# Kernel tuning notes

Hardware: AMD Instinct MI355X
Metric: run time of the kernel (lower is better)

## Reference

```python
import jax, jax.numpy as jnp
import numpy as np

B, QL, KVL = 4, 512, 4096
Q_DIM, KV_DIM = 1024, 768
QK_CH, V_CH, H = 1024, 1024, 8
DQK, DV = QK_CH // H, V_CH // H
LN_EPS = 1e-3  # keras LayerNormalization default epsilon


def layernorm(x, gamma, beta):
    mu = jnp.mean(x, axis=-1, keepdims=True)
    var = jnp.mean(jnp.square(x - mu), axis=-1, keepdims=True)
    return (x - mu) * jax.lax.rsqrt(var + LN_EPS) * gamma + beta


def setup_inputs() -> dict:
    key = jax.random.key(0)
    ks = jax.random.split(key, 8)
    s_q = 1.0 / np.sqrt(Q_DIM)
    s_kv = 1.0 / np.sqrt(KV_DIM)
    return {
        "hidden_states": jax.random.normal(ks[0], (B, QL, Q_DIM), jnp.float32),
        "inputs": jax.random.normal(ks[1], (B, KVL, KV_DIM), jnp.float32),
        "ln1_g": jnp.ones((Q_DIM,), jnp.float32),
        "ln1_b": jnp.zeros((Q_DIM,), jnp.float32),
        "ln2_g": jnp.ones((KV_DIM,), jnp.float32),
        "ln2_b": jnp.zeros((KV_DIM,), jnp.float32),
        "Wq": jax.random.normal(ks[2], (Q_DIM, QK_CH), jnp.float32) * s_q,
        "bq": jnp.zeros((QK_CH,), jnp.float32),
        "Wk": jax.random.normal(ks[3], (KV_DIM, QK_CH), jnp.float32) * s_kv,
        "bk": jnp.zeros((QK_CH,), jnp.float32),
        "Wv": jax.random.normal(ks[4], (KV_DIM, V_CH), jnp.float32) * s_kv,
        "bv": jnp.zeros((V_CH,), jnp.float32),
    }


def reference(hidden_states, inputs, ln1_g, ln1_b, ln2_g, ln2_b, Wq, bq, Wk, bk, Wv, bv):
    # LayerNorm latents and inputs (cross-attention path)
    hs = layernorm(hidden_states, ln1_g, ln1_b)   # [B, QL, Q_DIM]
    inp = layernorm(inputs, ln2_g, ln2_b)         # [B, KVL, KV_DIM]

    q = hs @ Wq + bq                               # [B, QL, QK_CH]
    k = inp @ Wk + bk                              # [B, KVL, QK_CH]
    v = inp @ Wv + bv                              # [B, KVL, V_CH]

    q = q.reshape(B, QL, H, DQK)
    k = k.reshape(B, KVL, H, DQK)
    v = v.reshape(B, KVL, H, DV)

    scores = jnp.einsum("bqhd,bkhd->bhqk", q, k) / jnp.sqrt(jnp.asarray(DQK, q.dtype))
    probs = jax.nn.softmax(scores, axis=-1)        # [B, H, QL, KVL]
    ctx = jnp.einsum("bhqk,bkhd->bqhd", probs, v)  # [B, QL, H, DV]
    return ctx.reshape(B, QL, H * DV)
```

## Files before the change

### kernel.cpp

```cpp
#include <hip/hip_runtime.h>
#include <hip/hip_bf16.h>
#include <stdint.h>

#define B_    4
#define QL_   512
#define KVL_  4096
#define QDIM  1024
#define KVDIM 768
#define NCH   1024
#define H_    8
#define DH    128
#define NROWS (B_ * H_ * QL_)
#define KVBLK 64
#define NS    4

typedef unsigned short ushort_t;
typedef __attribute__((ext_vector_type(8))) short bf16x8;
typedef __attribute__((ext_vector_type(4))) float f32x4;
typedef __attribute__((ext_vector_type(4))) unsigned short us4;

__device__ __forceinline__ ushort_t f2bf(float x){
  union { float f; unsigned u; } v; v.f = x;
  unsigned r = v.u + 0x7FFF + ((v.u >> 16) & 1);
  return (ushort_t)(r >> 16);
}

__device__ __forceinline__ void gload16(void* l, const void* g){
  __builtin_amdgcn_global_load_lds(
    (const __attribute__((address_space(1))) unsigned int*)g,
    (__attribute__((address_space(3))) unsigned int*)l, 16, 0, 0);
}

template<int D>
__global__ void ln_kernel(const float* __restrict__ x, const float* __restrict__ gamma,
                          const float* __restrict__ beta, ushort_t* __restrict__ out){
  int row = blockIdx.x;
  const float* xr = x + (size_t)row * D;
  ushort_t* orow = out + (size_t)row * D;
  int tid = threadIdx.x;
  constexpr int NPT = D / 256;
  float v[NPT];
  float s = 0.f, s2 = 0.f;
  #pragma unroll
  for (int k = 0; k < NPT; ++k){ v[k] = xr[tid + k*256]; s += v[k]; s2 += v[k]*v[k]; }
  #pragma unroll
  for (int m = 32; m; m >>= 1){ s += __shfl_xor(s, m); s2 += __shfl_xor(s2, m); }
  __shared__ float red[8];
  int w = tid >> 6;
  if ((tid & 63) == 0){ red[w] = s; red[4 + w] = s2; }
  __syncthreads();
  s  = red[0] + red[1] + red[2] + red[3];
  s2 = red[4] + red[5] + red[6] + red[7];
  float mu  = s / D;
  float var = s2 / D - mu * mu;
  float rs  = rsqrtf(var + 1e-3f);
  #pragma unroll
  for (int k = 0; k < NPT; ++k){
    int i = tid + k*256;
    orow[i] = f2bf((v[k] - mu) * rs * gamma[i] + beta[i]);
  }
}

__global__ void wtrans_kernel(const float* __restrict__ W, ushort_t* __restrict__ Wt,
                              int K, int N){
  __shared__ float t[32][33];
  int n0 = blockIdx.x * 32, k0 = blockIdx.y * 32;
  int tx = threadIdx.x & 31, ty = threadIdx.x >> 5;
  #pragma unroll
  for (int i = 0; i < 32; i += 8) t[ty + i][tx] = W[(size_t)(k0 + ty + i) * N + n0 + tx];
  __syncthreads();
  #pragma unroll
  for (int i = 0; i < 32; i += 8)
    Wt[(size_t)(n0 + ty + i) * K + k0 + tx] = f2bf(t[tx][ty + i]);
}

__global__ __launch_bounds__(256)
void gemm_kernel(const ushort_t* __restrict__ A, const ushort_t* __restrict__ Bw,
                 const float* __restrict__ bias, ushort_t* __restrict__ out,
                 int M, int K, float oscale){
  __shared__ __align__(16) ushort_t lds[3][2][4][128][8];
  int tid = threadIdx.x;
  int w = tid >> 6, lane = tid & 63;
  int m0 = blockIdx.x * 128, n0 = blockIdx.y * 128;
  int wr = w >> 1, wc = w & 1;
  int g = lane >> 4, j = lane & 15;
  f32x4 acc[4][4] = {};
  const int ksteps = K / 32;
  const ushort_t* Aw  = A  + (size_t)(m0 + lane) * K + w * 8;
  const ushort_t* Bww = Bw + (size_t)(n0 + lane) * K + w * 8;

  auto stage = [&](int buf, int ks){
    #pragma unroll
    for (int i = 0; i < 2; ++i){
      gload16(&lds[buf][0][w][i*64][0], Aw  + (size_t)i*64*K + ks*32);
      gload16(&lds[buf][1][w][i*64][0], Bww + (size_t)i*64*K + ks*32);
    }
  };

  stage(0, 0);
  stage(1, 1);
  asm volatile("s_waitcnt vmcnt(4)" ::: "memory");
  __builtin_amdgcn_s_barrier();
  __builtin_amdgcn_sched_barrier(0);

  int cur = 0;
  for (int ks = 0; ks < ksteps; ++ks){
    int nxt = cur + 2; if (nxt >= 3) nxt -= 3;
    bool pf = (ks + 2 < ksteps);
    if (pf) stage(nxt, ks + 2);
    bf16x8 af[4], bfr[4];
    #pragma unroll
    for (int mi = 0; mi < 4; ++mi) af[mi]  = *(const bf16x8*)&lds[cur][0][g][wr*64 + mi*16 + j][0];
    #pragma unroll
    for (int ni = 0; ni < 4; ++ni) bfr[ni] = *(const bf16x8*)&lds[cur][1][g][wc*64 + ni*16 + j][0];
    __builtin_amdgcn_s_setprio(1);
    #pragma unroll
    for (int mi = 0; mi < 4; ++mi)
      #pragma unroll
      for (int ni = 0; ni < 4; ++ni)
        acc[mi][ni] = __builtin_amdgcn_mfma_f32_16x16x32_bf16(af[mi], bfr[ni], acc[mi][ni], 0, 0, 0);
    __builtin_amdgcn_s_setprio(0);
    if (pf) asm volatile("s_waitcnt vmcnt(4)" ::: "memory");
    else    asm volatile("s_waitcnt vmcnt(0)" ::: "memory");
    __builtin_amdgcn_s_barrier();
    __builtin_amdgcn_sched_barrier(0);
    cur += 1; if (cur >= 3) cur -= 3;
  }

  #pragma unroll
  for (int mi = 0; mi < 4; ++mi){
    int row0 = m0 + wr*64 + mi*16 + g*4;
    #pragma unroll
    for (int ni = 0; ni < 4; ++ni){
      int col = n0 + wc*64 + ni*16 + j;
      float bs = bias[col];
      #pragma unroll
      for (int r = 0; r < 4; ++r)
        out[(size_t)(row0 + r) * NCH + col] = f2bf((acc[mi][ni][r] + bs) * oscale);
    }
  }
}

template<bool TRANSV>
__global__ __launch_bounds__(512, 2)
void gemm256_kernel(const ushort_t* __restrict__ A, const ushort_t* __restrict__ Bw,
                    const float* __restrict__ bias, ushort_t* __restrict__ out,
                    int M, int K, float oscale){
  __shared__ __align__(16) ushort_t lds[3][2][256][32];
  int tid = threadIdx.x;
  int w = tid >> 6, lane = tid & 63;
  int m0 = blockIdx.x * 256, n0 = blockIdx.y * 256;
  int wr = w >> 2, wc = w & 3;
  int g = lane >> 4, j = lane & 15;
  f32x4 acc[8][4] = {};
  const int ksteps = K / 32;
  int srow = tid >> 2, scolb = (tid & 3) * 8;
  const ushort_t* Asrc = A  + (size_t)(m0 + srow) * K + scolb;
  const ushort_t* Bsrc = Bw + (size_t)(n0 + srow) * K + scolb;

  auto stage = [&](int buf, int ks){
    char* la = (char*)&lds[buf][0][0][0] + tid * 16;
    char* lb = (char*)&lds[buf][1][0][0] + tid * 16;
    #pragma unroll
    for (int i = 0; i < 2; ++i){
      gload16(la + i*8192, Asrc + (size_t)(i*128)*K + ks*32);
      gload16(lb + i*8192, Bsrc + (size_t)(i*128)*K + ks*32);
    }
  };

  stage(0, 0);
  stage(1, 1);
  asm volatile("s_waitcnt vmcnt(4)" ::: "memory");
  __builtin_amdgcn_s_barrier();
  __builtin_amdgcn_sched_barrier(0);

  int cur = 0;
  for (int ks = 0; ks < ksteps; ++ks){
    int nxt = cur + 2; if (nxt >= 3) nxt -= 3;
    bool pf = (ks + 2 < ksteps);
    if (pf) stage(nxt, ks + 2);
    const char* La = (const char*)&lds[cur][0][0][0];
    const char* Lb = (const char*)&lds[cur][1][0][0];
    bf16x8 af[8], bfr[4];
    #pragma unroll
    for (int mi = 0; mi < 8; ++mi) af[mi]  = *(const bf16x8*)(La + ((wr*128 + mi*16 + j) << 6) + (g << 4));
    #pragma unroll
    for (int ni = 0; ni < 4; ++ni) bfr[ni] = *(const bf16x8*)(Lb + ((wc*64  + ni*16 + j) << 6) + (g << 4));
    __builtin_amdgcn_s_setprio(1);
    #pragma unroll
    for (int mi = 0; mi < 8; ++mi)
      #pragma unroll
      for (int ni = 0; ni < 4; ++ni)
        acc[mi][ni] = __builtin_amdgcn_mfma_f32_16x16x32_bf16(af[mi], bfr[ni], acc[mi][ni], 0, 0, 0);
    __builtin_amdgcn_s_setprio(0);
    if (pf) asm volatile("s_waitcnt vmcnt(4)" ::: "memory");
    else    asm volatile("s_waitcnt vmcnt(0)" ::: "memory");
    __builtin_amdgcn_s_barrier();
    __builtin_amdgcn_sched_barrier(0);
    cur += 1; if (cur >= 3) cur -= 3;
  }

  #pragma unroll
  for (int mi = 0; mi < 8; ++mi){
    int row0 = m0 + wr*128 + mi*16 + g*4;
    #pragma unroll
    for (int ni = 0; ni < 4; ++ni){
      int col = n0 + wc*64 + ni*16 + j;
      float bs = bias[col];
      if (!TRANSV){
        #pragma unroll
        for (int r = 0; r < 4; ++r)
          out[(size_t)(row0 + r) * NCH + col] = f2bf((acc[mi][ni][r] + bs) * oscale);
      } else {
        int bidx = row0 >> 12, kv = row0 & (KVL_ - 1);
        int h = col >> 7, dv = col & 127;
        int c = (kv & ~31) | (((kv & 15) >> 2) << 3) | (((kv >> 4) & 1) << 2);
        us4 pk;
        #pragma unroll
        for (int r = 0; r < 4; ++r) pk[r] = f2bf(acc[mi][ni][r] + bs);
        *(us4*)&out[((size_t)(bidx * H_ + h) * DH + dv) * KVL_ + c] = pk;
      }
    }
  }
}

__global__ __launch_bounds__(512, 4)
void attn_kernel(const ushort_t* __restrict__ Q, const ushort_t* __restrict__ Km,
                 const ushort_t* __restrict__ Vt, float* __restrict__ ctxp,
                 float* __restrict__ mlp){
  __shared__ __align__(16) ushort_t Kbuf[2][KVBLK][DH];
  __shared__ __align__(16) ushort_t Vbuf[2][DH][KVBLK];

  int bid = blockIdx.x;
  int xcd = bid & 7, slot = bid >> 3;
  int p   = xcd + 8 * (slot >> 2);
  int qb  = slot & 3;
  int bh  = p >> 2, sp = p & 3;
  int b = bh >> 3, h = bh & 7;

  int tid = threadIdx.x;
  int w = tid >> 6, lane = tid & 63;
  int g = lane >> 4, j = lane & 15;
  int qbase = qb * 128 + w * 16;

  bf16x8 qreg[4];
  {
    const ushort_t* Qb = Q + (size_t)(b * QL_ + qbase + j) * NCH + h * DH + g * 8;
    #pragma unroll
    for (int kb = 0; kb < 4; ++kb) qreg[kb] = *(const bf16x8*)(Qb + kb * 32);
  }

  f32x4 ctx[8] = {};
  float m_ = -1e30f, l_ = 0.f;

  const int kvbeg = sp * (KVL_ / NS);
  const char* Kg = (const char*)(Km + (size_t)b * KVL_ * NCH) + h * 256;
  const char* Vg = (const char*)(Vt + (size_t)(b * H_ + h) * DH * KVL_);

  auto stage = [&](int bi, int kv0){
    #pragma unroll
    for (int i = 0; i < 2; ++i){
      int lin = (i * 512 + tid) * 16;
      int sw  = lin ^ (((lin >> 8) & 7) << 4);
      gload16((char*)&Kbuf[bi][0][0] + lin,
              Kg + (size_t)(kv0 + (sw >> 8)) * 2048 + (sw & 255));
    }
    #pragma unroll
    for (int i = 0; i < 2; ++i){
      int lin = (i * 512 + tid) * 16;
      int sw  = lin ^ (((lin >> 7) & 7) << 4);
      gload16((char*)&Vbuf[bi][0][0] + lin,
              Vg + (size_t)(sw >> 7) * (KVL_ * 2) + kv0 * 2 + (sw & 127));
    }
  };

  const float THR = 11.5415603f;
  const int NCHUNK = (KVL_ / NS) / KVBLK;

  stage(0, kvbeg);
  __syncthreads();

  for (int c = 0; c < NCHUNK; ++c){
    int bi = c & 1;
    if (c + 1 < NCHUNK) stage(bi ^ 1, kvbeg + (c + 1) * KVBLK);

    const char* Kl = (const char*)&Kbuf[bi][0][0];
    const char* Vl = (const char*)&Vbuf[bi][0][0];

    f32x4 s[4] = {};
    __builtin_amdgcn_s_setprio(1);
    #pragma unroll
    for (int kf = 0; kf < 4; ++kf){
      #pragma unroll
      for (int kb = 0; kb < 4; ++kb){
        int off = (kf * 16 + j) * 256 + kb * 64 + g * 16;
        off ^= ((j & 7) << 4);
        s[kf] = __builtin_amdgcn_mfma_f32_16x16x32_bf16(
                  *(const bf16x8*)(Kl + off), qreg[kb], s[kf], 0, 0, 0);
      }
    }
    __builtin_amdgcn_s_setprio(0);

    float pm = s[0][0];
    #pragma unroll
    for (int kf = 0; kf < 4; ++kf)
      #pragma unroll
      for (int r = 0; r < 4; ++r) pm = fmaxf(pm, s[kf][r]);
    pm = fmaxf(pm, __shfl_xor(pm, 16));
    pm = fmaxf(pm, __shfl_xor(pm, 32));
    int ok = (pm - m_ <= THR);
    if (!__all(ok)){
      float mn = fmaxf(m_, pm);
      float cf = exp2f(m_ - mn);
      m_ = mn;
      l_ *= cf;
      float cfr[4];
      #pragma unroll
      for (int r = 0; r < 4; ++r) cfr[r] = __shfl(cf, g * 4 + r);
      #pragma unroll
      for (int df = 0; df < 8; ++df)
        #pragma unroll
        for (int r = 0; r < 4; ++r) ctx[df][r] *= cfr[r];
    }
    float rs = 0.f;
    #pragma unroll
    for (int kf = 0; kf < 4; ++kf)
      #pragma unroll
      for (int r = 0; r < 4; ++r){ s[kf][r] = exp2f(s[kf][r] - m_); rs += s[kf][r]; }
    rs += __shfl_xor(rs, 16);
    rs += __shfl_xor(rs, 32);
    l_ += rs;

    union { unsigned u[4]; bf16x8 v; } pa[2];
    #pragma unroll
    for (int kb = 0; kb < 2; ++kb){
      asm("v_cvt_pk_bf16_f32 %0, %1, %2" : "=v"(pa[kb].u[0]) : "v"(s[2*kb][0]),   "v"(s[2*kb][1]));
      asm("v_cvt_pk_bf16_f32 %0, %1, %2" : "=v"(pa[kb].u[1]) : "v"(s[2*kb][2]),   "v"(s[2*kb][3]));
      asm("v_cvt_pk_bf16_f32 %0, %1, %2" : "=v"(pa[kb].u[2]) : "v"(s[2*kb+1][0]), "v"(s[2*kb+1][1]));
      asm("v_cvt_pk_bf16_f32 %0, %1, %2" : "=v"(pa[kb].u[3]) : "v"(s[2*kb+1][2]), "v"(s[2*kb+1][3]));
    }

    __builtin_amdgcn_s_setprio(1);
    #pragma unroll
    for (int df = 0; df < 8; ++df){
      int off0 = (df * 16 + j) * 128 + g * 16;        int o0 = off0 ^ ((j & 7) << 4);
      int off1 = (df * 16 + j) * 128 + 64 + g * 16;   int o1 = off1 ^ ((j & 7) << 4);
      ctx[df] = __builtin_amdgcn_mfma_f32_16x16x32_bf16(pa[0].v, *(const bf16x8*)(Vl + o0), ctx[df], 0, 0, 0);
      ctx[df] = __builtin_amdgcn_mfma_f32_16x16x32_bf16(pa[1].v, *(const bf16x8*)(Vl + o1), ctx[df], 0, 0, 0);
    }
    __builtin_amdgcn_s_setprio(0);
    __syncthreads();
  }

  size_t prow0 = ((size_t)sp * 32 + bh) * QL_ + qbase;
  #pragma unroll
  for (int r = 0; r < 4; ++r){
    float* cp = ctxp + (prow0 + g * 4 + r) * DH;
    #pragma unroll
    for (int df = 0; df < 8; ++df) cp[df * 16 + j] = ctx[df][r];
  }
  if (g == 0){
    mlp[(prow0 + j) * 2]     = m_;
    mlp[(prow0 + j) * 2 + 1] = l_;
  }
}

__global__ __launch_bounds__(256)
void combine_kernel(const float* __restrict__ ctxp, const float* __restrict__ mlp,
                    float* __restrict__ out){
  int row = blockIdx.x * 4 + (threadIdx.x >> 6);
  int lane = threadIdx.x & 63;
  int b = row >> 12, h = (row >> 9) & 7, q = row & 511;
  float ms[NS], ls[NS];
  #pragma unroll
  for (int s = 0; s < NS; ++s){
    ms[s] = mlp[((size_t)(s * NROWS + row)) * 2];
    ls[s] = mlp[((size_t)(s * NROWS + row)) * 2 + 1];
  }
  float M = ms[0];
  #pragma unroll
  for (int s = 1; s < NS; ++s) M = fmaxf(M, ms[s]);
  float wgt[NS], L = 0.f;
  #pragma unroll
  for (int s = 0; s < NS; ++s){ wgt[s] = exp2f(ms[s] - M); L += ls[s] * wgt[s]; }
  float inv = 1.f / L;
  float ax = 0.f, ay = 0.f;
  #pragma unroll
  for (int s = 0; s < NS; ++s){
    const float* cp = ctxp + ((size_t)(s * NROWS + row)) * DH + lane * 2;
    ax += cp[0] * wgt[s]; ay += cp[1] * wgt[s];
  }
  float* op = out + ((size_t)(b * QL_ + q)) * NCH + h * DH + lane * 2;
  op[0] = ax * inv; op[1] = ay * inv;
}

extern "C" void kernel_launch(void* const* d_in, const int* in_sizes, int n_in,
                              void* d_out, int out_size, void* d_ws, size_t ws_size,
                              hipStream_t stream){
  const float* hs   = (const float*)d_in[0];
  const float* inp  = (const float*)d_in[1];
  const float* ln1g = (const float*)d_in[2];
  const float* ln1b = (const float*)d_in[3];
  const float* ln2g = (const float*)d_in[4];
  const float* ln2b = (const float*)d_in[5];
  const float* Wq   = (const float*)d_in[6];
  const float* bq   = (const float*)d_in[7];
  const float* Wk   = (const float*)d_in[8];
  const float* bk   = (const float*)d_in[9];
  const float* Wv   = (const float*)d_in[10];
  const float* bv   = (const float*)d_in[11];

  char* ws = (char*)d_ws;
  size_t off = 0;
  auto alloc = [&](size_t bytes){ void* pp = ws + off; off += (bytes + 255) & ~255ull; return pp; };
  ushort_t* Qm = (ushort_t*)alloc((size_t)2048 * 1024 * 2);
  ushort_t* Km = (ushort_t*)alloc((size_t)16384 * 1024 * 2);
  ushort_t* Vt = (ushort_t*)alloc((size_t)16384 * 1024 * 2);
  size_t base2 = off;
  ushort_t* hs_ln = (ushort_t*)alloc((size_t)2048 * 1024 * 2);
  ushort_t* in_ln = (ushort_t*)alloc((size_t)16384 * 768 * 2);
  ushort_t* Wqt   = (ushort_t*)alloc((size_t)1024 * 1024 * 2);
  ushort_t* Wkt   = (ushort_t*)alloc((size_t)1024 * 768 * 2);
  ushort_t* Wvt   = (ushort_t*)alloc((size_t)1024 * 768 * 2);
  off = base2;
  float* ctxp = (float*)alloc((size_t)NS * NROWS * DH * 4);
  float* mlp  = (float*)alloc((size_t)NS * NROWS * 2 * 4);

  const float QSC = 0.08838834764831845f * 1.4426950408889634f;

  ln_kernel<1024><<<2048, 256, 0, stream>>>(hs, ln1g, ln1b, hs_ln);
  ln_kernel<768><<<16384, 256, 0, stream>>>(inp, ln2g, ln2b, in_ln);
  wtrans_kernel<<<dim3(32, 32), 256, 0, stream>>>(Wq, Wqt, 1024, 1024);
  wtrans_kernel<<<dim3(32, 24), 256, 0, stream>>>(Wk, Wkt, 768, 1024);
  wtrans_kernel<<<dim3(32, 24), 256, 0, stream>>>(Wv, Wvt, 768, 1024);
  gemm_kernel<<<dim3(16, 8), 256, 0, stream>>>(hs_ln, Wqt, bq, Qm, 2048, 1024, QSC);
  gemm256_kernel<false><<<dim3(64, 4), 512, 0, stream>>>(in_ln, Wkt, bk, Km, 16384, 768, 1.0f);
  gemm256_kernel<true ><<<dim3(64, 4), 512, 0, stream>>>(in_ln, Wvt, bv, Vt, 16384, 768, 1.0f);
  attn_kernel<<<512, 512, 0, stream>>>(Qm, Km, Vt, ctxp, mlp);
  combine_kernel<<<NROWS / 4, 256, 0, stream>>>(ctxp, mlp, (float*)d_out);
}
```

Before: 175.3 us.

## Give each attention wave two query tiles and vectorize layernorm loads

The attention kernel drops from 512 to 256 threads per block, and each wave now handles two 16-row query groups. Each K and V fragment read from LDS is reused across two MFMAs, which halves LDS read traffic per unit of work. The cost is more registers per wave (two sets of ctx accumulators and softmax state) and fewer waves to hide latency. Separately, the layernorm kernel now does float4 loads and a packed bf16 store, with block size set to D/4 threads.

Result: no change. 176.4 us (+0.6%).

```diff
diff --git a/kernel.cpp b/kernel.cpp
--- a/kernel.cpp
+++ b/kernel.cpp
@@ -34,31 +34,31 @@
 template<int D>
 __global__ void ln_kernel(const float* __restrict__ x, const float* __restrict__ gamma,
                           const float* __restrict__ beta, ushort_t* __restrict__ out){
+  constexpr int NW = D / 256;
   int row = blockIdx.x;
-  const float* xr = x + (size_t)row * D;
-  ushort_t* orow = out + (size_t)row * D;
+  const f32x4* xr = (const f32x4*)(x + (size_t)row * D);
   int tid = threadIdx.x;
-  constexpr int NPT = D / 256;
-  float v[NPT];
-  float s = 0.f, s2 = 0.f;
-  #pragma unroll
-  for (int k = 0; k < NPT; ++k){ v[k] = xr[tid + k*256]; s += v[k]; s2 += v[k]*v[k]; }
+  f32x4 v = xr[tid];
+  float s  = v[0] + v[1] + v[2] + v[3];
+  float s2 = v[0]*v[0] + v[1]*v[1] + v[2]*v[2] + v[3]*v[3];
   #pragma unroll
   for (int m = 32; m; m >>= 1){ s += __shfl_xor(s, m); s2 += __shfl_xor(s2, m); }
-  __shared__ float red[8];
+  __shared__ float red[2 * NW];
   int w = tid >> 6;
-  if ((tid & 63) == 0){ red[w] = s; red[4 + w] = s2; }
+  if ((tid & 63) == 0){ red[w] = s; red[NW + w] = s2; }
   __syncthreads();
-  s  = red[0] + red[1] + red[2] + red[3];
-  s2 = red[4] + red[5] + red[6] + red[7];
+  s = 0.f; s2 = 0.f;
+  #pragma unroll
+  for (int i = 0; i < NW; ++i){ s += red[i]; s2 += red[NW + i]; }
   float mu  = s / D;
   float var = s2 / D - mu * mu;
   float rs  = rsqrtf(var + 1e-3f);
-  #pragma unroll
-  for (int k = 0; k < NPT; ++k){
-    int i = tid + k*256;
-    orow[i] = f2bf((v[k] - mu) * rs * gamma[i] + beta[i]);
-  }
+  f32x4 gm = ((const f32x4*)gamma)[tid];
+  f32x4 bt = ((const f32x4*)beta)[tid];
+  us4 o;
+  #pragma unroll
+  for (int e = 0; e < 4; ++e) o[e] = f2bf((v[e] - mu) * rs * gm[e] + bt[e]);
+  ((us4*)(out + (size_t)row * D))[tid] = o;
 }
 
 __global__ void wtrans_kernel(const float* __restrict__ W, ushort_t* __restrict__ Wt,
@@ -224,7 +224,7 @@
   }
 }
 
-__global__ __launch_bounds__(512, 4)
+__global__ __launch_bounds__(256, 2)
 void attn_kernel(const ushort_t* __restrict__ Q, const ushort_t* __restrict__ Km,
                  const ushort_t* __restrict__ Vt, float* __restrict__ ctxp,
                  float* __restrict__ mlp){
@@ -241,17 +241,18 @@
   int tid = threadIdx.x;
   int w = tid >> 6, lane = tid & 63;
   int g = lane >> 4, j = lane & 15;
-  int qbase = qb * 128 + w * 16;
-
-  bf16x8 qreg[4];
-  {
-    const ushort_t* Qb = Q + (size_t)(b * QL_ + qbase + j) * NCH + h * DH + g * 8;
-    #pragma unroll
-    for (int kb = 0; kb < 4; ++kb) qreg[kb] = *(const bf16x8*)(Qb + kb * 32);
-  }
-
-  f32x4 ctx[8] = {};
-  float m_ = -1e30f, l_ = 0.f;
+  int qbase = qb * 128 + w * 32;
+
+  bf16x8 qreg[2][4];
+  #pragma unroll
+  for (int qg = 0; qg < 2; ++qg){
+    const ushort_t* Qb = Q + (size_t)(b * QL_ + qbase + qg * 16 + j) * NCH + h * DH + g * 8;
+    #pragma unroll
+    for (int kb = 0; kb < 4; ++kb) qreg[qg][kb] = *(const bf16x8*)(Qb + kb * 32);
+  }
+
+  f32x4 ctx[2][8] = {};
+  float m_[2] = {-1e30f, -1e30f}, l_[2] = {0.f, 0.f};
 
   const int kvbeg = sp * (KVL_ / NS);
   const char* Kg = (const char*)(Km + (size_t)b * KVL_ * NCH) + h * 256;
@@ -259,15 +260,15 @@
 
   auto stage = [&](int bi, int kv0){
     #pragma unroll
-    for (int i = 0; i < 2; ++i){
-      int lin = (i * 512 + tid) * 16;
+    for (int i = 0; i < 4; ++i){
+      int lin = (i * 256 + tid) * 16;
       int sw  = lin ^ (((lin >> 8) & 7) << 4);
       gload16((char*)&Kbuf[bi][0][0] + lin,
               Kg + (size_t)(kv0 + (sw >> 8)) * 2048 + (sw & 255));
     }
     #pragma unroll
-    for (int i = 0; i < 2; ++i){
-      int lin = (i * 512 + tid) * 16;
+    for (int i = 0; i < 4; ++i){
+      int lin = (i * 256 + tid) * 16;
       int sw  = lin ^ (((lin >> 7) & 7) << 4);
       gload16((char*)&Vbuf[bi][0][0] + lin,
               Vg + (size_t)(sw >> 7) * (KVL_ * 2) + kv0 * 2 + (sw & 127));
@@ -287,7 +288,7 @@
     const char* Kl = (const char*)&Kbuf[bi][0][0];
     const char* Vl = (const char*)&Vbuf[bi][0][0];
 
-    f32x4 s[4] = {};
+    f32x4 s[2][4] = {};
     __builtin_amdgcn_s_setprio(1);
     #pragma unroll
     for (int kf = 0; kf < 4; ++kf){
@@ -295,49 +296,56 @@
       for (int kb = 0; kb < 4; ++kb){
         int off = (kf * 16 + j) * 256 + kb * 64 + g * 16;
         off ^= ((j & 7) << 4);
-        s[kf] = __builtin_amdgcn_mfma_f32_16x16x32_bf16(
-                  *(const bf16x8*)(Kl + off), qreg[kb], s[kf], 0, 0, 0);
+        bf16x8 kfrag = *(const bf16x8*)(Kl + off);
+        s[0][kf] = __builtin_amdgcn_mfma_f32_16x16x32_bf16(kfrag, qreg[0][kb], s[0][kf], 0, 0, 0);
+        s[1][kf] = __builtin_amdgcn_mfma_f32_16x16x32_bf16(kfrag, qreg[1][kb], s[1][kf], 0, 0, 0);
       }
     }
     __builtin_amdgcn_s_setprio(0);
 
-    float pm = s[0][0];
-    #pragma unroll
-    for (int kf = 0; kf < 4; ++kf)
-      #pragma unroll
-      for (int r = 0; r < 4; ++r) pm = fmaxf(pm, s[kf][r]);
-    pm = fmaxf(pm, __shfl_xor(pm, 16));
-    pm = fmaxf(pm, __shfl_xor(pm, 32));
-    int ok = (pm - m_ <= THR);
-    if (!__all(ok)){
-      float mn = fmaxf(m_, pm);
-      float cf = exp2f(m_ - mn);
-      m_ = mn;
-      l_ *= cf;
-      float cfr[4];
-      #pragma unroll
-      for (int r = 0; r < 4; ++r) cfr[r] = __shfl(cf, g * 4 + r);
-      #pragma unroll
-      for (int df = 0; df < 8; ++df)
+    union { unsigned u[4]; bf16x8 v; } pa[2][2];
+    #pragma unroll
+    for (int qg = 0; qg < 2; ++qg){
+      float t0 = fmaxf(fmaxf(s[qg][0][0], s[qg][0][1]), fmaxf(s[qg][0][2], s[qg][0][3]));
+      float t1 = fmaxf(fmaxf(s[qg][1][0], s[qg][1][1]), fmaxf(s[qg][1][2], s[qg][1][3]));
+      float t2 = fmaxf(fmaxf(s[qg][2][0], s[qg][2][1]), fmaxf(s[qg][2][2], s[qg][2][3]));
+      float t3 = fmaxf(fmaxf(s[qg][3][0], s[qg][3][1]), fmaxf(s[qg][3][2], s[qg][3][3]));
+      float pm = fmaxf(fmaxf(t0, t1), fmaxf(t2, t3));
+      pm = fmaxf(pm, __shfl_xor(pm, 16));
+      pm = fmaxf(pm, __shfl_xor(pm, 32));
+      int ok = (pm - m_[qg] <= THR);
+      if (!__all(ok)){
+        float mn = fmaxf(m_[qg], pm);
+        float cf = exp2f(m_[qg] - mn);
+        m_[qg] = mn;
+        l_[qg] *= cf;
+        float cfr[4];
         #pragma unroll
-        for (int r = 0; r < 4; ++r) ctx[df][r] *= cfr[r];
-    }
-    float rs = 0.f;
-    #pragma unroll
-    for (int kf = 0; kf < 4; ++kf)
-      #pragma unroll
-      for (int r = 0; r < 4; ++r){ s[kf][r] = exp2f(s[kf][r] - m_); rs += s[kf][r]; }
-    rs += __shfl_xor(rs, 16);
-    rs += __shfl_xor(rs, 32);
-    l_ += rs;
-
-    union { unsigned u[4]; bf16x8 v; } pa[2];
-    #pragma unroll
-    for (int kb = 0; kb < 2; ++kb){
-      asm("v_cvt_pk_bf16_f32 %0, %1, %2" : "=v"(pa[kb].u[0]) : "v"(s[2*kb][0]),   "v"(s[2*kb][1]));
-      asm("v_cvt_pk_bf16_f32 %0, %1, %2" : "=v"(pa[kb].u[1]) : "v"(s[2*kb][2]),   "v"(s[2*kb][3]));
-      asm("v_cvt_pk_bf16_f32 %0, %1, %2" : "=v"(pa[kb].u[2]) : "v"(s[2*kb+1][0]), "v"(s[2*kb+1][1]));
-      asm("v_cvt_pk_bf16_f32 %0, %1, %2" : "=v"(pa[kb].u[3]) : "v"(s[2*kb+1][2]), "v"(s[2*kb+1][3]));
+        for (int r = 0; r < 4; ++r) cfr[r] = __shfl(cf, g * 4 + r);
+        #pragma unroll
+        for (int df = 0; df < 8; ++df)
+          #pragma unroll
+          for (int r = 0; r < 4; ++r) ctx[qg][df][r] *= cfr[r];
+      }
+      float rs0 = 0.f, rs1 = 0.f;
+      #pragma unroll
+      for (int kf = 0; kf < 4; ++kf)
+        #pragma unroll
+        for (int r = 0; r < 4; ++r){
+          s[qg][kf][r] = exp2f(s[qg][kf][r] - m_[qg]);
+          if (kf < 2) rs0 += s[qg][kf][r]; else rs1 += s[qg][kf][r];
+        }
+      float rs = rs0 + rs1;
+      rs += __shfl_xor(rs, 16);
+      rs += __shfl_xor(rs, 32);
+      l_[qg] += rs;
+      #pragma unroll
+      for (int kb = 0; kb < 2; ++kb){
+        asm("v_cvt_pk_bf16_f32 %0, %1, %2" : "=v"(pa[qg][kb].u[0]) : "v"(s[qg][2*kb][0]),   "v"(s[qg][2*kb][1]));
+        asm("v_cvt_pk_bf16_f32 %0, %1, %2" : "=v"(pa[qg][kb].u[1]) : "v"(s[qg][2*kb][2]),   "v"(s[qg][2*kb][3]));
+        asm("v_cvt_pk_bf16_f32 %0, %1, %2" : "=v"(pa[qg][kb].u[2]) : "v"(s[qg][2*kb+1][0]), "v"(s[qg][2*kb+1][1]));
+        asm("v_cvt_pk_bf16_f32 %0, %1, %2" : "=v"(pa[qg][kb].u[3]) : "v"(s[qg][2*kb+1][2]), "v"(s[qg][2*kb+1][3]));
+      }
     }
 
     __builtin_amdgcn_s_setprio(1);
@@ -345,23 +353,30 @@
     for (int df = 0; df < 8; ++df){
       int off0 = (df * 16 + j) * 128 + g * 16;        int o0 = off0 ^ ((j & 7) << 4);
       int off1 = (df * 16 + j) * 128 + 64 + g * 16;   int o1 = off1 ^ ((j & 7) << 4);
-      ctx[df] = __builtin_amdgcn_mfma_f32_16x16x32_bf16(pa[0].v, *(const bf16x8*)(Vl + o0), ctx[df], 0, 0, 0);
-      ctx[df] = __builtin_amdgcn_mfma_f32_16x16x32_bf16(pa[1].v, *(const bf16x8*)(Vl + o1), ctx[df], 0, 0, 0);
+      bf16x8 v0 = *(const bf16x8*)(Vl + o0);
+      bf16x8 v1 = *(const bf16x8*)(Vl + o1);
+      ctx[0][df] = __builtin_amdgcn_mfma_f32_16x16x32_bf16(pa[0][0].v, v0, ctx[0][df], 0, 0, 0);
+      ctx[0][df] = __builtin_amdgcn_mfma_f32_16x16x32_bf16(pa[0][1].v, v1, ctx[0][df], 0, 0, 0);
+      ctx[1][df] = __builtin_amdgcn_mfma_f32_16x16x32_bf16(pa[1][0].v, v0, ctx[1][df], 0, 0, 0);
+      ctx[1][df] = __builtin_amdgcn_mfma_f32_16x16x32_bf16(pa[1][1].v, v1, ctx[1][df], 0, 0, 0);
     }
     __builtin_amdgcn_s_setprio(0);
     __syncthreads();
   }
 
-  size_t prow0 = ((size_t)sp * 32 + bh) * QL_ + qbase;
-  #pragma unroll
-  for (int r = 0; r < 4; ++r){
-    float* cp = ctxp + (prow0 + g * 4 + r) * DH;
-    #pragma unroll
-    for (int df = 0; df < 8; ++df) cp[df * 16 + j] = ctx[df][r];
-  }
-  if (g == 0){
-    mlp[(prow0 + j) * 2]     = m_;
-    mlp[(prow0 + j) * 2 + 1] = l_;
+  #pragma unroll
+  for (int qg = 0; qg < 2; ++qg){
+    size_t prow0 = ((size_t)sp * 32 + bh) * QL_ + qbase + qg * 16;
+    #pragma unroll
+    for (int r = 0; r < 4; ++r){
+      float* cp = ctxp + (prow0 + g * 4 + r) * DH;
+      #pragma unroll
+      for (int df = 0; df < 8; ++df) cp[df * 16 + j] = ctx[qg][df][r];
+    }
+    if (g == 0){
+      mlp[(prow0 + j) * 2]     = m_[qg];
+      mlp[(prow0 + j) * 2 + 1] = l_[qg];
+    }
   }
 }
 
@@ -429,13 +444,13 @@
   const float QSC = 0.08838834764831845f * 1.4426950408889634f;
 
   ln_kernel<1024><<<2048, 256, 0, stream>>>(hs, ln1g, ln1b, hs_ln);
-  ln_kernel<768><<<16384, 256, 0, stream>>>(inp, ln2g, ln2b, in_ln);
+  ln_kernel<768><<<16384, 192, 0, stream>>>(inp, ln2g, ln2b, in_ln);
   wtrans_kernel<<<dim3(32, 32), 256, 0, stream>>>(Wq, Wqt, 1024, 1024);
   wtrans_kernel<<<dim3(32, 24), 256, 0, stream>>>(Wk, Wkt, 768, 1024);
   wtrans_kernel<<<dim3(32, 24), 256, 0, stream>>>(Wv, Wvt, 768, 1024);
   gemm_kernel<<<dim3(16, 8), 256, 0, stream>>>(hs_ln, Wqt, bq, Qm, 2048, 1024, QSC);
   gemm256_kernel<false><<<dim3(64, 4), 512, 0, stream>>>(in_ln, Wkt, bk, Km, 16384, 768, 1.0f);
   gemm256_kernel<true ><<<dim3(64, 4), 512, 0, stream>>>(in_ln, Wvt, bv, Vt, 16384, 768, 1.0f);
-  attn_kernel<<<512, 512, 0, stream>>>(Qm, Km, Vt, ctxp, mlp);
+  attn_kernel<<<512, 256, 0, stream>>>(Qm, Km, Vt, ctxp, mlp);
   combine_kernel<<<NROWS / 4, 256, 0, stream>>>(ctxp, mlp, (float*)d_out);
 }
```
